# Kernel tuning notes

Measured on AMD Instinct MI355X. Metric: run time of the kernel, lower is better.

The kernel has to match this reference:

```python
import jax, jax.numpy as jnp
import numpy as np

N, B, C, H = 1024, 4, 1024, 8
D = C // H  # head dim = 128


def setup_inputs() -> dict:
    key = jax.random.key(0)
    ks = jax.random.split(key, 10)
    f = lambda k, s: jax.random.normal(k, s, dtype=jnp.float32)
    w = lambda k: f(k, (C, C)) * 0.02  # torch Linear weight layout (out, in)
    return {
        "query_reg": f(ks[0], (N, B, C)),
        "key_reg": f(ks[1], (N, B, C)),
        "query_cls": f(ks[2], (N, B, C)),
        "key_cls": f(ks[3], (N, B, C)),
        "value": f(ks[4], (N, B, C)),
        "W_q_reg": w(ks[5]),
        "W_k_reg": w(ks[6]),
        "W_q_cls": w(ks[7]),
        "W_k_cls": w(ks[8]),
        "W_v": w(ks[9]),
    }


def _proj_heads(x, W):
    # x: (N, B, C); torch Linear: y = x @ W.T -> reshape (N,B,H,D) -> (B,H,N,D)
    y = jnp.einsum('nbc,dc->nbd', x, W)
    return y.reshape(N, B, H, D).transpose(1, 2, 0, 3)


def _l2norm(x):
    return x / jnp.linalg.norm(x, axis=-1, keepdims=True)


def reference(query_reg, key_reg, query_cls, key_cls, value,
              W_q_reg, W_k_reg, W_q_cls, W_k_cls, W_v):
    q_reg = _l2norm(_proj_heads(query_reg, W_q_reg))  # (B,H,N,D)
    k_reg = _l2norm(_proj_heads(key_reg, W_k_reg))
    q_cls = _l2norm(_proj_heads(query_cls, W_q_cls))
    k_cls = _l2norm(_proj_heads(key_cls, W_k_cls))
    v = _proj_heads(value, W_v)

    attn_reg = jax.nn.softmax(jnp.einsum('bhnd,bhmd->bhnm', q_reg, k_reg), axis=-1)
    attn_cls = jax.nn.softmax(jnp.einsum('bhnd,bhmd->bhnm', q_cls, k_cls), axis=-1)
    attn = (attn_reg + attn_cls) * 0.5  # (B,H,N,N)

    x = jnp.einsum('bhnm,bhmd->bhnd', attn, v)  # (B,H,N,D)
    x = x.transpose(0, 2, 1, 3).reshape(B, N, C)  # (B,N,C)
    return (x.transpose(1, 0, 2), attn)  # ((N,B,C), (B,H,N,N))
```

## Files before the change

kernel.cpp:

```cpp
#include <hip/hip_runtime.h>

#define DEVINL __device__ __forceinline__

typedef unsigned short u16;
typedef float f32x4 __attribute__((ext_vector_type(4)));
typedef __bf16 bf16x8 __attribute__((ext_vector_type(8)));

constexpr int N_ = 1024, B_ = 4, C_ = 1024, H_ = 8, D_ = 128;
constexpr int NB = N_ * B_;
constexpr int BH = B_ * H_;

DEVINL u16 f2bf(float f) {
  unsigned u = __builtin_bit_cast(unsigned, f);
  u += 0x7fffu + ((u >> 16) & 1u);
  return (u16)(u >> 16);
}
DEVINL float bf2f(u16 v) { return __builtin_bit_cast(float, ((unsigned)v) << 16); }

typedef __attribute__((address_space(1))) void gv_t;
typedef __attribute__((address_space(3))) void lv_t;
DEVINL void gload16(const void* g, void* l) {
  __builtin_amdgcn_global_load_lds((gv_t*)(unsigned long long)g,
                                   (lv_t*)(unsigned)(unsigned long long)l, 16, 0, 0);
}
DEVINL bf16x8 ld_frag(const u16* p) { return *(const bf16x8*)p; }
DEVINL f32x4 mfma16(bf16x8 a, bf16x8 b, f32x4 c) {
  return __builtin_amdgcn_mfma_f32_16x16x32_bf16(a, b, c, 0, 0, 0);
}

struct ConvArgs { const float* s[10]; u16* d[10]; int n[10]; };

__global__ __launch_bounds__(256) void k_convert(ConvArgs a) {
  const int which = blockIdx.y;
  const int i = (blockIdx.x * 256 + threadIdx.x) * 8;
  if (i >= a.n[which]) return;
  const float* s = a.s[which] + i;
  float4 v0 = *(const float4*)s;
  float4 v1 = *(const float4*)(s + 4);
  union { uint4 v; u16 r[8]; } u;
  u.r[0] = f2bf(v0.x); u.r[1] = f2bf(v0.y); u.r[2] = f2bf(v0.z); u.r[3] = f2bf(v0.w);
  u.r[4] = f2bf(v1.x); u.r[5] = f2bf(v1.y); u.r[6] = f2bf(v1.z); u.r[7] = f2bf(v1.w);
  *(uint4*)(a.d[which] + i) = u.v;
}

struct ProjArgs { const u16* X[5]; const u16* W[5]; u16* O[5]; };

__global__ __launch_bounds__(256) void k_proj(ProjArgs a) {
  __shared__ u16 lA[128 * 64];
  __shared__ u16 lB[128 * 64];
  __shared__ float lred[128][2];
  const int tid = threadIdx.x, w = tid >> 6, lane = tid & 63;
  const int qd = lane >> 4, m16 = lane & 15;
  const int wr = w >> 1, wc = w & 1;
  const int r0 = blockIdx.y * 128, d0 = blockIdx.x * 128;
  const u16* __restrict__ X = a.X[blockIdx.z];
  const u16* __restrict__ W = a.W[blockIdx.z];
  u16* __restrict__ O = a.O[blockIdx.z];
  const bool donorm = blockIdx.z < 4;

  f32x4 acc[4][4];
  const f32x4 fz = {0.f, 0.f, 0.f, 0.f};
#pragma unroll
  for (int i = 0; i < 4; ++i)
#pragma unroll
    for (int j = 0; j < 4; ++j) acc[i][j] = fz;

  for (int k0 = 0; k0 < C_; k0 += 64) {
    __syncthreads();
#pragma unroll
    for (int i = 0; i < 4; ++i) {
      int p = i * 256 + tid, row = p >> 3, cp = p & 7, cl = cp ^ (row & 7);
      gload16(X + (size_t)(r0 + row) * C_ + k0 + cl * 8, &lA[p * 8]);
    }
#pragma unroll
    for (int i = 0; i < 4; ++i) {
      int p = i * 256 + tid, row = p >> 3, cp = p & 7, cl = cp ^ (row & 7);
      gload16(W + (size_t)(d0 + row) * C_ + k0 + cl * 8, &lB[p * 8]);
    }
    __syncthreads();
#pragma unroll
    for (int ks = 0; ks < 2; ++ks) {
      bf16x8 af[4], bfr[4];
#pragma unroll
      for (int t = 0; t < 4; ++t) {
        int row = wr * 64 + t * 16 + m16;
        af[t] = ld_frag(&lA[row * 64 + (((ks * 4 + qd) ^ (row & 7)) * 8)]);
        int col = wc * 64 + t * 16 + m16;
        bfr[t] = ld_frag(&lB[col * 64 + (((ks * 4 + qd) ^ (col & 7)) * 8)]);
      }
#pragma unroll
      for (int rt = 0; rt < 4; ++rt)
#pragma unroll
        for (int ct = 0; ct < 4; ++ct)
          acc[rt][ct] = mfma16(af[rt], bfr[ct], acc[rt][ct]);
    }
  }
  if (donorm) {
    float s[4][4];
#pragma unroll
    for (int rt = 0; rt < 4; ++rt)
#pragma unroll
      for (int rg = 0; rg < 4; ++rg) {
        float t = 0.f;
#pragma unroll
        for (int ct = 0; ct < 4; ++ct) t += acc[rt][ct][rg] * acc[rt][ct][rg];
        s[rt][rg] = t;
      }
#pragma unroll
    for (int off = 1; off < 16; off <<= 1)
#pragma unroll
      for (int rt = 0; rt < 4; ++rt)
#pragma unroll
        for (int rg = 0; rg < 4; ++rg) s[rt][rg] += __shfl_xor(s[rt][rg], off);
    if (m16 == 0) {
#pragma unroll
      for (int rt = 0; rt < 4; ++rt)
#pragma unroll
        for (int rg = 0; rg < 4; ++rg)
          lred[wr * 64 + rt * 16 + qd * 4 + rg][wc] = s[rt][rg];
    }
  }
  __syncthreads();
  float inv[4][4];
#pragma unroll
  for (int rt = 0; rt < 4; ++rt)
#pragma unroll
    for (int rg = 0; rg < 4; ++rg) {
      if (donorm) {
        int row = wr * 64 + rt * 16 + qd * 4 + rg;
        inv[rt][rg] = rsqrtf(lred[row][0] + lred[row][1]);
      } else inv[rt][rg] = 1.0f;
    }
#pragma unroll
  for (int rt = 0; rt < 4; ++rt)
#pragma unroll
    for (int ct = 0; ct < 4; ++ct)
#pragma unroll
      for (int rg = 0; rg < 4; ++rg) {
        int row = r0 + wr * 64 + rt * 16 + qd * 4 + rg;
        int col = d0 + wc * 64 + ct * 16 + m16;
        int n = row >> 2, b = row & 3, h = col >> 7, d = col & 127;
        O[(((size_t)(b * H_ + h)) * N_ + n) * D_ + d] = f2bf(acc[rt][ct][rg] * inv[rt][rg]);
      }
}

__global__ __launch_bounds__(256) void k_transpose(const u16* __restrict__ v,
                                                   u16* __restrict__ vt) {
  __shared__ u16 tile[128][65];
  const int bh = blockIdx.y, n0 = blockIdx.x * 64;
  const u16* src = v + (size_t)bh * N_ * D_;
  u16* dst = vt + (size_t)bh * D_ * N_;
  union U8 { uint4 v; u16 s[8]; };
#pragma unroll
  for (int it = 0; it < 4; ++it) {
    int c = it * 256 + threadIdx.x;
    int n = c >> 4, dc = (c & 15) * 8;
    U8 u; u.v = *(const uint4*)(src + (size_t)(n0 + n) * D_ + dc);
#pragma unroll
    for (int j = 0; j < 8; ++j) tile[dc + j][n] = u.s[j];
  }
  __syncthreads();
#pragma unroll
  for (int it = 0; it < 4; ++it) {
    int c = it * 256 + threadIdx.x;
    int d = c >> 3, nc = (c & 7) * 8;
    U8 u;
#pragma unroll
    for (int j = 0; j < 8; ++j) u.s[j] = tile[d][nc + j];
    *(uint4*)(dst + (size_t)d * N_ + n0 + nc) = u.v;
  }
}

__global__ __launch_bounds__(512, 2) void k_attn(const u16* __restrict__ qr,
                                                 const u16* __restrict__ kr,
                                                 const u16* __restrict__ qc,
                                                 const u16* __restrict__ kc,
                                                 const u16* __restrict__ vt,
                                                 float* __restrict__ out0,
                                                 float* __restrict__ out1) {
  __shared__ u16 lK[2][2][128 * 128];
  __shared__ u16 lP[2][32 * 136];
  __shared__ float lred[2][8][32];
  const int flat = blockIdx.x + (blockIdx.y << 5);
  const int xcd = flat & 7, kk = flat >> 3;
  const int bh = (xcd << 2) + (kk >> 5);
  const int n0 = (kk & 31) * 32;
  const int b = bh >> 3, h = bh & 7;
  const size_t base = (size_t)bh * N_ * D_;
  const int tid = threadIdx.x, w = tid >> 6, lane = tid & 63;
  const int qd = lane >> 4, m16 = lane & 15;
  const u16* ksrc[2] = {kr, kc};

  bf16x8 qf[2][2][4];
#pragma unroll
  for (int ct = 0; ct < 2; ++ct)
#pragma unroll
    for (int ks = 0; ks < 4; ++ks) {
      size_t ro = base + (size_t)(n0 + ct * 16 + m16) * D_ + ks * 32 + qd * 8;
      qf[0][ct][ks] = ld_frag(qr + ro);
      qf[1][ct][ks] = ld_frag(qc + ro);
    }

  uint2 pst[2][8][2];
  float psum[2][2] = {{0.f, 0.f}, {0.f, 0.f}};
  const f32x4 fz = {0.f, 0.f, 0.f, 0.f};

#pragma unroll
  for (int ty = 0; ty < 2; ++ty)
#pragma unroll
    for (int i = 0; i < 4; ++i) {
      int p = i * 512 + tid, row = p >> 4, cp = p & 15, cl = cp ^ (row & 15);
      gload16(ksrc[ty] + base + (size_t)row * D_ + cl * 8, &lK[0][ty][p * 8]);
    }
  __syncthreads();

#pragma unroll
  for (int mt = 0; mt < 8; ++mt) {
    const int cur = mt & 1;
    if (mt < 7) {
      const int m0n = (mt + 1) * 128;
#pragma unroll
      for (int ty = 0; ty < 2; ++ty)
#pragma unroll
        for (int i = 0; i < 4; ++i) {
          int p = i * 512 + tid, row = p >> 4, cp = p & 15, cl = cp ^ (row & 15);
          gload16(ksrc[ty] + base + (size_t)(m0n + row) * D_ + cl * 8,
                  &lK[cur ^ 1][ty][p * 8]);
        }
    }
    const int mrow = w * 16 + m16;
#pragma unroll
    for (int ty = 0; ty < 2; ++ty) {
      bf16x8 af[4];
#pragma unroll
      for (int ks = 0; ks < 4; ++ks)
        af[ks] = ld_frag(&lK[cur][ty][mrow * 128 + (((ks * 4 + qd) ^ (mrow & 15)) * 8)]);
#pragma unroll
      for (int ct = 0; ct < 2; ++ct) {
        f32x4 acc = fz;
#pragma unroll
        for (int ks = 0; ks < 4; ++ks) acc = mfma16(af[ks], qf[ty][ct][ks], acc);
        union { uint2 u; u16 s[4]; } pk;
        float loc = 0.f;
#pragma unroll
        for (int rg = 0; rg < 4; ++rg) {
          float e = __expf(acc[rg]);
          loc += e;
          pk.s[rg] = f2bf(e);
        }
        psum[ty][ct] += loc;
        pst[ty][mt][ct] = pk.u;
      }
    }
    __syncthreads();
  }

#pragma unroll
  for (int ty = 0; ty < 2; ++ty)
#pragma unroll
    for (int ct = 0; ct < 2; ++ct) {
      psum[ty][ct] += __shfl_xor(psum[ty][ct], 16);
      psum[ty][ct] += __shfl_xor(psum[ty][ct], 32);
    }
  if (qd == 0) {
#pragma unroll
    for (int ty = 0; ty < 2; ++ty)
#pragma unroll
      for (int ct = 0; ct < 2; ++ct) lred[ty][w][ct * 16 + m16] = psum[ty][ct];
  }
  __syncthreads();
  float il[2][2];
#pragma unroll
  for (int ty = 0; ty < 2; ++ty)
#pragma unroll
    for (int ct = 0; ct < 2; ++ct) {
      int n = ct * 16 + m16;
      float s = 0.f;
#pragma unroll
      for (int ww = 0; ww < 8; ++ww) s += lred[ty][ww][n];
      il[ty][ct] = 0.5f / s;
    }

  f32x4 xacc[2] = {fz, fz};
  float* attn = out1 + (size_t)bh * N_ * N_;
  const u16* vtb = vt + (size_t)bh * D_ * N_ + (size_t)(w * 16 + m16) * N_;

#pragma unroll
  for (int mt = 0; mt < 8; ++mt) {
    const int cur = mt & 1;
    const int m0 = mt * 128;
#pragma unroll
    for (int ct = 0; ct < 2; ++ct) {
      union { uint2 u; u16 s[4]; } ur, uc, pk;
      ur.u = pst[0][mt][ct];
      uc.u = pst[1][mt][ct];
      f32x4 pv;
#pragma unroll
      for (int rg = 0; rg < 4; ++rg) {
        pv[rg] = bf2f(ur.s[rg]) * il[0][ct] + bf2f(uc.s[rg]) * il[1][ct];
        pk.s[rg] = f2bf(pv[rg]);
      }
      const int nrow = n0 + ct * 16 + m16;
      const int mcol = m0 + w * 16 + qd * 4;
      *(f32x4*)(attn + (size_t)nrow * N_ + mcol) = pv;
      *(uint2*)&lP[cur][(ct * 16 + m16) * 136 + w * 16 + qd * 4] = pk.u;
    }
    __syncthreads();
#pragma unroll
    for (int ks = 0; ks < 4; ++ks) {
      bf16x8 pa[2];
#pragma unroll
      for (int ct = 0; ct < 2; ++ct)
        pa[ct] = ld_frag(&lP[cur][(ct * 16 + m16) * 136 + ks * 32 + qd * 8]);
      bf16x8 vb = ld_frag(vtb + m0 + ks * 32 + qd * 8);
#pragma unroll
      for (int ct = 0; ct < 2; ++ct)
        xacc[ct] = mfma16(pa[ct], vb, xacc[ct]);
    }
  }
#pragma unroll
  for (int ct = 0; ct < 2; ++ct)
#pragma unroll
    for (int rg = 0; rg < 4; ++rg) {
      int n = n0 + ct * 16 + qd * 4 + rg;
      int d = w * 16 + m16;
      out0[((size_t)n * B_ + b) * C_ + h * 128 + d] = xacc[ct][rg];
    }
}

extern "C" void kernel_launch(void* const* d_in, const int* in_sizes, int n_in,
                              void* d_out, int out_size, void* d_ws, size_t ws_size,
                              hipStream_t stream) {
  (void)in_sizes; (void)n_in; (void)out_size; (void)ws_size;
  const float* in_f[10];
  for (int i = 0; i < 10; ++i) in_f[i] = (const float*)d_in[i];

  u16* ws = (u16*)d_ws;
  u16* Xc[5], *Wc[5], *P[5];
  for (int i = 0; i < 5; ++i) Xc[i] = ws + (size_t)i * NB * C_;
  u16* wbase = ws + (size_t)5 * NB * C_;
  for (int i = 0; i < 5; ++i) Wc[i] = wbase + (size_t)i * C_ * C_;
  u16* pbase = wbase + (size_t)5 * C_ * C_;
  for (int i = 0; i < 5; ++i) P[i] = pbase + (size_t)i * BH * N_ * D_;
  u16* vt = pbase + (size_t)5 * BH * N_ * D_;

  float* out0 = (float*)d_out;
  float* out1 = out0 + (size_t)N_ * B_ * C_;

  ConvArgs ca;
  for (int i = 0; i < 5; ++i) { ca.s[i] = in_f[i];     ca.d[i] = Xc[i];  ca.n[i] = NB * C_; }
  for (int i = 0; i < 5; ++i) { ca.s[5+i] = in_f[5+i]; ca.d[5+i] = Wc[i]; ca.n[5+i] = C_ * C_; }
  k_convert<<<dim3(2048, 10), 256, 0, stream>>>(ca);

  ProjArgs pa;
  for (int i = 0; i < 5; ++i) { pa.X[i] = Xc[i]; pa.W[i] = Wc[i]; pa.O[i] = P[i]; }
  k_proj<<<dim3(C_ / 128, NB / 128, 5), 256, 0, stream>>>(pa);

  k_transpose<<<dim3(N_ / 64, BH), 256, 0, stream>>>(P[4], vt);

  k_attn<<<dim3(N_ / 32, BH), 512, 0, stream>>>(P[0], P[1], P[2], P[3], vt, out0, out1);
}
```

Measured before the change: 392.3 us.

## Fuse PV into score loop with deferred normalization, swizzle proj blocks, nontemporal stores

The attention kernel now multiplies unnormalized exp-scores for each branch by V inside the first K pass, keeping separate accumulators for the reg and cls branches. Normalization by the row sums is applied at the end, which removes the second pass's dependence on an LDS round trip for P·V. The attn matrix is written afterwards with nontemporal stores and s_setprio hints are added around the MFMA sections. Separately, the projection kernel remaps block indices into an XCD-aware order. Risks are higher register pressure from doubled accumulators and extra LDS syncs per tile.

Result: slower. 412.3 us (+5.1%).

```diff
diff --git a/kernel.cpp b/kernel.cpp
--- a/kernel.cpp
+++ b/kernel.cpp
@@ -52,11 +52,14 @@
   const int tid = threadIdx.x, w = tid >> 6, lane = tid & 63;
   const int qd = lane >> 4, m16 = lane & 15;
   const int wr = w >> 1, wc = w & 1;
-  const int r0 = blockIdx.y * 128, d0 = blockIdx.x * 128;
-  const u16* __restrict__ X = a.X[blockIdx.z];
-  const u16* __restrict__ W = a.W[blockIdx.z];
-  u16* __restrict__ O = a.O[blockIdx.z];
-  const bool donorm = blockIdx.z < 4;
+  const int flat = blockIdx.x + (blockIdx.y << 3) + (blockIdx.z << 8);
+  const int swz = (flat & 7) * 160 + (flat >> 3);
+  const int bz = swz >> 8, rem = swz & 255, by = rem >> 3, bx = rem & 7;
+  const int r0 = by * 128, d0 = bx * 128;
+  const u16* __restrict__ X = a.X[bz];
+  const u16* __restrict__ W = a.W[bz];
+  u16* __restrict__ O = a.O[bz];
+  const bool donorm = bz < 4;
 
   f32x4 acc[4][4];
   const f32x4 fz = {0.f, 0.f, 0.f, 0.f};
@@ -181,6 +184,7 @@
   __shared__ u16 lK[2][2][128 * 128];
   __shared__ u16 lP[2][32 * 136];
   __shared__ float lred[2][8][32];
+  __shared__ float dsum[2][32];
   const int flat = blockIdx.x + (blockIdx.y << 5);
   const int xcd = flat & 7, kk = flat >> 3;
   const int bh = (xcd << 2) + (kk >> 5);
@@ -204,6 +208,12 @@
   uint2 pst[2][8][2];
   float psum[2][2] = {{0.f, 0.f}, {0.f, 0.f}};
   const f32x4 fz = {0.f, 0.f, 0.f, 0.f};
+  f32x4 xacc[2][2];
+#pragma unroll
+  for (int ty = 0; ty < 2; ++ty)
+#pragma unroll
+    for (int ct = 0; ct < 2; ++ct) xacc[ty][ct] = fz;
+  const u16* vtb = vt + (size_t)bh * D_ * N_ + (size_t)(w * 16 + m16) * N_;
 
 #pragma unroll
   for (int ty = 0; ty < 2; ++ty)
@@ -217,6 +227,7 @@
 #pragma unroll
   for (int mt = 0; mt < 8; ++mt) {
     const int cur = mt & 1;
+    const int m0 = mt * 128;
     if (mt < 7) {
       const int m0n = (mt + 1) * 128;
 #pragma unroll
@@ -228,7 +239,13 @@
                   &lK[cur ^ 1][ty][p * 8]);
         }
     }
+    bf16x8 vb[4];
+#pragma unroll
+    for (int ks = 0; ks < 4; ++ks)
+      vb[ks] = ld_frag(vtb + m0 + ks * 32 + qd * 8);
+
     const int mrow = w * 16 + m16;
+    __builtin_amdgcn_s_setprio(1);
 #pragma unroll
     for (int ty = 0; ty < 2; ++ty) {
       bf16x8 af[4];
@@ -250,8 +267,27 @@
         }
         psum[ty][ct] += loc;
         pst[ty][mt][ct] = pk.u;
+        *(uint2*)&lP[ty][(ct * 16 + m16) * 136 + w * 16 + qd * 4] = pk.u;
       }
     }
+    __builtin_amdgcn_s_setprio(0);
+    __syncthreads();
+    __builtin_amdgcn_s_setprio(1);
+#pragma unroll
+    for (int ks = 0; ks < 4; ++ks) {
+      bf16x8 pa[2][2];
+#pragma unroll
+      for (int ty = 0; ty < 2; ++ty)
+#pragma unroll
+        for (int ct = 0; ct < 2; ++ct)
+          pa[ty][ct] = ld_frag(&lP[ty][(ct * 16 + m16) * 136 + ks * 32 + qd * 8]);
+#pragma unroll
+      for (int ty = 0; ty < 2; ++ty)
+#pragma unroll
+        for (int ct = 0; ct < 2; ++ct)
+          xacc[ty][ct] = mfma16(pa[ty][ct], vb[ks], xacc[ty][ct]);
+    }
+    __builtin_amdgcn_s_setprio(0);
     __syncthreads();
   }
 
@@ -269,63 +305,51 @@
       for (int ct = 0; ct < 2; ++ct) lred[ty][w][ct * 16 + m16] = psum[ty][ct];
   }
   __syncthreads();
-  float il[2][2];
-#pragma unroll
-  for (int ty = 0; ty < 2; ++ty)
+  if (tid < 64) {
+    int ty = tid >> 5, n = tid & 31;
+    float s = 0.f;
+#pragma unroll
+    for (int ww = 0; ww < 8; ++ww) s += lred[ty][ww][n];
+    dsum[ty][n] = s;
+  }
+  __syncthreads();
+
+#pragma unroll
+  for (int ct = 0; ct < 2; ++ct)
+#pragma unroll
+    for (int rg = 0; rg < 4; ++rg) {
+      int nn = ct * 16 + qd * 4 + rg;
+      float i0 = 0.5f / dsum[0][nn];
+      float i1 = 0.5f / dsum[1][nn];
+      int n = n0 + nn;
+      int d = w * 16 + m16;
+      float val = xacc[0][ct][rg] * i0 + xacc[1][ct][rg] * i1;
+      __builtin_nontemporal_store(val, &out0[((size_t)n * B_ + b) * C_ + h * 128 + d]);
+    }
+
+  float il0[2], il1[2];
+#pragma unroll
+  for (int ct = 0; ct < 2; ++ct) {
+    il0[ct] = 0.5f / dsum[0][ct * 16 + m16];
+    il1[ct] = 0.5f / dsum[1][ct * 16 + m16];
+  }
+  float* attn = out1 + (size_t)bh * N_ * N_;
+#pragma unroll
+  for (int mt = 0; mt < 8; ++mt) {
 #pragma unroll
     for (int ct = 0; ct < 2; ++ct) {
-      int n = ct * 16 + m16;
-      float s = 0.f;
-#pragma unroll
-      for (int ww = 0; ww < 8; ++ww) s += lred[ty][ww][n];
-      il[ty][ct] = 0.5f / s;
-    }
-
-  f32x4 xacc[2] = {fz, fz};
-  float* attn = out1 + (size_t)bh * N_ * N_;
-  const u16* vtb = vt + (size_t)bh * D_ * N_ + (size_t)(w * 16 + m16) * N_;
-
-#pragma unroll
-  for (int mt = 0; mt < 8; ++mt) {
-    const int cur = mt & 1;
-    const int m0 = mt * 128;
-#pragma unroll
-    for (int ct = 0; ct < 2; ++ct) {
-      union { uint2 u; u16 s[4]; } ur, uc, pk;
+      union { uint2 u; u16 s[4]; } ur, uc;
       ur.u = pst[0][mt][ct];
       uc.u = pst[1][mt][ct];
       f32x4 pv;
 #pragma unroll
-      for (int rg = 0; rg < 4; ++rg) {
-        pv[rg] = bf2f(ur.s[rg]) * il[0][ct] + bf2f(uc.s[rg]) * il[1][ct];
-        pk.s[rg] = f2bf(pv[rg]);
-      }
+      for (int rg = 0; rg < 4; ++rg)
+        pv[rg] = bf2f(ur.s[rg]) * il0[ct] + bf2f(uc.s[rg]) * il1[ct];
       const int nrow = n0 + ct * 16 + m16;
-      const int mcol = m0 + w * 16 + qd * 4;
-      *(f32x4*)(attn + (size_t)nrow * N_ + mcol) = pv;
-      *(uint2*)&lP[cur][(ct * 16 + m16) * 136 + w * 16 + qd * 4] = pk.u;
-    }
-    __syncthreads();
-#pragma unroll
-    for (int ks = 0; ks < 4; ++ks) {
-      bf16x8 pa[2];
-#pragma unroll
-      for (int ct = 0; ct < 2; ++ct)
-        pa[ct] = ld_frag(&lP[cur][(ct * 16 + m16) * 136 + ks * 32 + qd * 8]);
-      bf16x8 vb = ld_frag(vtb + m0 + ks * 32 + qd * 8);
-#pragma unroll
-      for (int ct = 0; ct < 2; ++ct)
-        xacc[ct] = mfma16(pa[ct], vb, xacc[ct]);
-    }
-  }
-#pragma unroll
-  for (int ct = 0; ct < 2; ++ct)
-#pragma unroll
-    for (int rg = 0; rg < 4; ++rg) {
-      int n = n0 + ct * 16 + qd * 4 + rg;
-      int d = w * 16 + m16;
-      out0[((size_t)n * B_ + b) * C_ + h * 128 + d] = xacc[ct][rg];
-    }
+      const int mcol = mt * 128 + w * 16 + qd * 4;
+      __builtin_nontemporal_store(pv, (f32x4*)(attn + (size_t)nrow * N_ + mcol));
+    }
+  }
 }
 
 extern "C" void kernel_launch(void* const* d_in, const int* in_sizes, int n_in,
```

## Fuse V transpose into projection, swizzle blocks, coalesce nontemporal attn stores

Applied to the files above, without the earlier changes.

The V projection now writes its output already transposed into the vt buffer through an LDS staging tile, which removes the separate transpose kernel launch. Projection blocks are remapped with an XCD-aware swizzle to improve L2 locality. In the attention kernel the fp32 attention matrix is now written from the bf16 P tile in LDS as row-contiguous 32-byte nontemporal stores instead of scattered 16-byte stores. The stored attention values become bf16-rounded, a small precision loss.

Result: slower. 427.3 us (+8.9%).

```diff
diff --git a/kernel.cpp b/kernel.cpp
--- a/kernel.cpp
+++ b/kernel.cpp
@@ -46,17 +46,21 @@
 struct ProjArgs { const u16* X[5]; const u16* W[5]; u16* O[5]; };
 
 __global__ __launch_bounds__(256) void k_proj(ProjArgs a) {
-  __shared__ u16 lA[128 * 64];
-  __shared__ u16 lB[128 * 64];
+  __shared__ u16 sAB[2 * 128 * 64];
   __shared__ float lred[128][2];
+  u16* const lA = sAB;
+  u16* const lB = sAB + 128 * 64;
   const int tid = threadIdx.x, w = tid >> 6, lane = tid & 63;
   const int qd = lane >> 4, m16 = lane & 15;
   const int wr = w >> 1, wc = w & 1;
-  const int r0 = blockIdx.y * 128, d0 = blockIdx.x * 128;
-  const u16* __restrict__ X = a.X[blockIdx.z];
-  const u16* __restrict__ W = a.W[blockIdx.z];
-  u16* __restrict__ O = a.O[blockIdx.z];
-  const bool donorm = blockIdx.z < 4;
+  const int flat = blockIdx.x + (blockIdx.y << 3) + (blockIdx.z << 8);
+  const int swz = (flat & 7) * 160 + (flat >> 3);
+  const int bz = swz >> 8, rem = swz & 255, by = rem >> 3, bx = rem & 7;
+  const int r0 = by * 128, d0 = bx * 128;
+  const u16* __restrict__ X = a.X[bz];
+  const u16* __restrict__ W = a.W[bz];
+  u16* __restrict__ O = a.O[bz];
+  const bool donorm = bz < 4;
 
   f32x4 acc[4][4];
   const f32x4 fz = {0.f, 0.f, 0.f, 0.f};
@@ -121,53 +125,50 @@
     }
   }
   __syncthreads();
-  float inv[4][4];
-#pragma unroll
-  for (int rt = 0; rt < 4; ++rt)
-#pragma unroll
-    for (int rg = 0; rg < 4; ++rg) {
-      if (donorm) {
+
+  if (donorm) {
+    float inv[4][4];
+#pragma unroll
+    for (int rt = 0; rt < 4; ++rt)
+#pragma unroll
+      for (int rg = 0; rg < 4; ++rg) {
         int row = wr * 64 + rt * 16 + qd * 4 + rg;
         inv[rt][rg] = rsqrtf(lred[row][0] + lred[row][1]);
-      } else inv[rt][rg] = 1.0f;
-    }
-#pragma unroll
-  for (int rt = 0; rt < 4; ++rt)
-#pragma unroll
-    for (int ct = 0; ct < 4; ++ct)
-#pragma unroll
-      for (int rg = 0; rg < 4; ++rg) {
-        int row = r0 + wr * 64 + rt * 16 + qd * 4 + rg;
-        int col = d0 + wc * 64 + ct * 16 + m16;
-        int n = row >> 2, b = row & 3, h = col >> 7, d = col & 127;
-        O[(((size_t)(b * H_ + h)) * N_ + n) * D_ + d] = f2bf(acc[rt][ct][rg] * inv[rt][rg]);
-      }
-}
-
-__global__ __launch_bounds__(256) void k_transpose(const u16* __restrict__ v,
-                                                   u16* __restrict__ vt) {
-  __shared__ u16 tile[128][65];
-  const int bh = blockIdx.y, n0 = blockIdx.x * 64;
-  const u16* src = v + (size_t)bh * N_ * D_;
-  u16* dst = vt + (size_t)bh * D_ * N_;
-  union U8 { uint4 v; u16 s[8]; };
-#pragma unroll
-  for (int it = 0; it < 4; ++it) {
-    int c = it * 256 + threadIdx.x;
-    int n = c >> 4, dc = (c & 15) * 8;
-    U8 u; u.v = *(const uint4*)(src + (size_t)(n0 + n) * D_ + dc);
-#pragma unroll
-    for (int j = 0; j < 8; ++j) tile[dc + j][n] = u.s[j];
-  }
-  __syncthreads();
-#pragma unroll
-  for (int it = 0; it < 4; ++it) {
-    int c = it * 256 + threadIdx.x;
-    int d = c >> 3, nc = (c & 7) * 8;
-    U8 u;
-#pragma unroll
-    for (int j = 0; j < 8; ++j) u.s[j] = tile[d][nc + j];
-    *(uint4*)(dst + (size_t)d * N_ + n0 + nc) = u.v;
+      }
+#pragma unroll
+    for (int rt = 0; rt < 4; ++rt)
+#pragma unroll
+      for (int ct = 0; ct < 4; ++ct)
+#pragma unroll
+        for (int rg = 0; rg < 4; ++rg) {
+          int row = r0 + wr * 64 + rt * 16 + qd * 4 + rg;
+          int col = d0 + wc * 64 + ct * 16 + m16;
+          int n = row >> 2, b = row & 3, h = col >> 7, d = col & 127;
+          O[(((size_t)(b * H_ + h)) * N_ + n) * D_ + d] = f2bf(acc[rt][ct][rg] * inv[rt][rg]);
+        }
+  } else {
+    u16 (*lT)[136] = (u16(*)[136])sAB;
+    const int hh = bx;
+    const int nb0 = r0 >> 2;
+#pragma unroll
+    for (int hp = 0; hp < 2; ++hp) {
+      if (hp) __syncthreads();
+      if (wc == hp) {
+#pragma unroll
+        for (int rt = 0; rt < 4; ++rt)
+#pragma unroll
+          for (int ct = 0; ct < 4; ++ct)
+#pragma unroll
+            for (int rg = 0; rg < 4; ++rg)
+              lT[ct * 16 + m16][rg * 32 + wr * 16 + rt * 4 + qd] = f2bf(acc[rt][ct][rg]);
+      }
+      __syncthreads();
+      const int dl = tid >> 2, bb = tid & 3;
+      u16* dst = O + ((size_t)(bb * H_ + hh) * D_ + hp * 64 + dl) * N_ + nb0;
+#pragma unroll
+      for (int j = 0; j < 4; ++j)
+        *(uint4*)(dst + j * 8) = *(const uint4*)&lT[dl][bb * 32 + j * 8];
+    }
   }
 }
 
@@ -284,6 +285,8 @@
   f32x4 xacc[2] = {fz, fz};
   float* attn = out1 + (size_t)bh * N_ * N_;
   const u16* vtb = vt + (size_t)bh * D_ * N_ + (size_t)(w * 16 + m16) * N_;
+  const int en = tid >> 4;
+  const int em = (tid & 15) * 8;
 
 #pragma unroll
   for (int mt = 0; mt < 8; ++mt) {
@@ -294,18 +297,22 @@
       union { uint2 u; u16 s[4]; } ur, uc, pk;
       ur.u = pst[0][mt][ct];
       uc.u = pst[1][mt][ct];
-      f32x4 pv;
-#pragma unroll
-      for (int rg = 0; rg < 4; ++rg) {
-        pv[rg] = bf2f(ur.s[rg]) * il[0][ct] + bf2f(uc.s[rg]) * il[1][ct];
-        pk.s[rg] = f2bf(pv[rg]);
-      }
-      const int nrow = n0 + ct * 16 + m16;
-      const int mcol = m0 + w * 16 + qd * 4;
-      *(f32x4*)(attn + (size_t)nrow * N_ + mcol) = pv;
+#pragma unroll
+      for (int rg = 0; rg < 4; ++rg)
+        pk.s[rg] = f2bf(bf2f(ur.s[rg]) * il[0][ct] + bf2f(uc.s[rg]) * il[1][ct]);
       *(uint2*)&lP[cur][(ct * 16 + m16) * 136 + w * 16 + qd * 4] = pk.u;
     }
     __syncthreads();
+    {
+      union { uint4 v; u16 s[8]; } pr;
+      pr.v = *(const uint4*)&lP[cur][en * 136 + em];
+      f32x4 lo, hi;
+#pragma unroll
+      for (int j = 0; j < 4; ++j) { lo[j] = bf2f(pr.s[j]); hi[j] = bf2f(pr.s[4 + j]); }
+      float* ap = attn + (size_t)(n0 + en) * N_ + m0 + em;
+      __builtin_nontemporal_store(lo, (f32x4*)ap);
+      __builtin_nontemporal_store(hi, (f32x4*)(ap + 4));
+    }
 #pragma unroll
     for (int ks = 0; ks < 4; ++ks) {
       bf16x8 pa[2];
@@ -354,9 +361,8 @@
 
   ProjArgs pa;
   for (int i = 0; i < 5; ++i) { pa.X[i] = Xc[i]; pa.W[i] = Wc[i]; pa.O[i] = P[i]; }
+  pa.O[4] = vt;
   k_proj<<<dim3(C_ / 128, NB / 128, 5), 256, 0, stream>>>(pa);
 
-  k_transpose<<<dim3(N_ / 64, BH), 256, 0, stream>>>(P[4], vt);
-
   k_attn<<<dim3(N_ / 32, BH), 512, 0, stream>>>(P[0], P[1], P[2], P[3], vt, out0, out1);
 }
```
